# Kernel optimization log

Hardware: AMD Instinct MI355X
Metric: run time of the kernel (lower is better)

## Reference

```python
import jax, jax.numpy as jnp
import numpy as np

D_MODEL = 2048
NUM_HEADS = 16
HEAD_DIM = D_MODEL // NUM_HEADS
BATCH = 2
SEQ = 2048


def setup_inputs() -> dict:
    key = jax.random.key(0)
    ks = jax.random.split(key, 5)
    scale = 1.0 / np.sqrt(D_MODEL)
    x = jax.random.normal(ks[0], (BATCH, SEQ, D_MODEL), dtype=jnp.float32)
    wq = jax.random.normal(ks[1], (D_MODEL, D_MODEL), dtype=jnp.float32) * scale
    wk = jax.random.normal(ks[2], (D_MODEL, D_MODEL), dtype=jnp.float32) * scale
    wv = jax.random.normal(ks[3], (D_MODEL, D_MODEL), dtype=jnp.float32) * scale
    wo = jax.random.normal(ks[4], (D_MODEL, D_MODEL), dtype=jnp.float32) * scale
    return {"x": x, "wq": wq, "wk": wk, "wv": wv, "wo": wo}


def reference(x, wq, wk, wv, wo):
    # x: [B, S, D_MODEL]; torch nn.Linear(bias=False): y = x @ W.T
    B, S, _ = x.shape

    def split_heads(t):
        # [B, S, D] -> [B, H, S, Dh]
        return t.reshape(B, S, NUM_HEADS, HEAD_DIM).transpose(0, 2, 1, 3)

    q = split_heads(x @ wq.T)
    k = split_heads(x @ wk.T)
    v = split_heads(x @ wv.T)

    # scaled dot-product attention with causal (tril) mask, single-rank path
    scores = jnp.einsum("bhqd,bhkd->bhqk", q, k) / jnp.sqrt(
        jnp.asarray(HEAD_DIM, dtype=x.dtype)
    )
    causal = jnp.tril(jnp.ones((S, S), dtype=bool))  # [S, S]
    neg_inf = jnp.asarray(jnp.finfo(scores.dtype).min, dtype=scores.dtype)
    scores = jnp.where(causal[None, None, :, :], scores, neg_inf)
    attn = jax.nn.softmax(scores, axis=-1)

    out = jnp.einsum("bhqk,bhkd->bhqd", attn, v)  # [B, H, S, Dh]
    out = out.transpose(0, 2, 1, 3).reshape(B, S, D_MODEL)
    return out @ wo.T
```

## Files before the change

### kernel.cpp

```cpp
#include <hip/hip_runtime.h>
#include <hip/hip_bf16.h>

#define D_MODEL   2048
#define NUM_HEADS 16
#define HEAD_DIM  128
#define BATCH     2
#define SEQ       2048

typedef short bf16x8 __attribute__((ext_vector_type(8)));
typedef float f32x4  __attribute__((ext_vector_type(4)));

__device__ inline short f2bf(float x) {
    __hip_bfloat16 h = __float2bfloat16(x);
    return *reinterpret_cast<short*>(&h);
}

__device__ inline void async_copy16(const void* g, void* l) {
    __builtin_amdgcn_global_load_lds(
        (const __attribute__((address_space(1))) void*)g,
        (__attribute__((address_space(3))) void*)l, 16, 0, 0);
}
__device__ inline void wait_all() { __builtin_amdgcn_s_waitcnt(0); }

__global__ __launch_bounds__(256) void f32_to_bf16(
    const float* __restrict__ src, __hip_bfloat16* __restrict__ dst, int n8) {
    const int i = blockIdx.x * 256 + threadIdx.x;
    if (i >= n8) return;
    const f32x4* p = (const f32x4*)src + (size_t)i * 2;
    f32x4 f0 = p[0], f1 = p[1];
    bf16x8 v;
#pragma unroll
    for (int j = 0; j < 4; ++j) { v[j] = f2bf(f0[j]); v[4 + j] = f2bf(f1[j]); }
    *(bf16x8*)((short*)dst + (size_t)i * 8) = v;
}

__global__ __launch_bounds__(256) void cvt5(
    const float* __restrict__ x,  __hip_bfloat16* __restrict__ xb,
    const float* __restrict__ w0, __hip_bfloat16* __restrict__ w0b,
    const float* __restrict__ w1, __hip_bfloat16* __restrict__ w1b,
    const float* __restrict__ w2, __hip_bfloat16* __restrict__ w2b,
    const float* __restrict__ w3, __hip_bfloat16* __restrict__ w3b) {
    const int b = blockIdx.x;
    const float* src; short* dst; int idx;
    if (b < 4096)       { src = x;  dst = (short*)xb;  idx = b; }
    else if (b < 6144)  { src = w0; dst = (short*)w0b; idx = b - 4096; }
    else if (b < 8192)  { src = w1; dst = (short*)w1b; idx = b - 6144; }
    else if (b < 10240) { src = w2; dst = (short*)w2b; idx = b - 8192; }
    else                { src = w3; dst = (short*)w3b; idx = b - 10240; }
    const int i = idx * 256 + threadIdx.x;
    const f32x4* p = (const f32x4*)src + (size_t)i * 2;
    f32x4 f0 = p[0], f1 = p[1];
    bf16x8 v;
#pragma unroll
    for (int j = 0; j < 4; ++j) { v[j] = f2bf(f0[j]); v[4 + j] = f2bf(f1[j]); }
    *(bf16x8*)(dst + (size_t)i * 8) = v;
}

template <bool OUT_F32>
__global__ __launch_bounds__(256) void gemm_v4(
    const __hip_bfloat16* __restrict__ A,
    const __hip_bfloat16* __restrict__ W0,
    const __hip_bfloat16* __restrict__ W1,
    const __hip_bfloat16* __restrict__ W2,
    void* __restrict__ C0, void* __restrict__ C1, void* __restrict__ C2,
    int M, int N, int K) {
    __shared__ short As[2][128 * 64];
    __shared__ short Ws[2][128 * 64];

    const int z = blockIdx.z;
    const __hip_bfloat16* W = (z == 0) ? W0 : (z == 1) ? W1 : W2;
    void* Cv = (z == 0) ? C0 : (z == 1) ? C1 : C2;

    const int gx  = gridDim.x;
    const int nwg = gx * gridDim.y;
    const int wg  = blockIdx.y * gx + blockIdx.x;
    const int swz = (wg & 7) * (nwg >> 3) + (wg >> 3);
    const int bx  = swz % gx;
    const int by  = swz / gx;

    const int tid  = threadIdx.x;
    const int lane = tid & 63;
    const int wv   = tid >> 6;
    const int c    = lane & 15;
    const int quad = lane >> 4;
    const int m0   = by * 128;
    const int n0   = bx * 128;
    const int wm   = (wv >> 1) * 64;
    const int wn   = (wv & 1) * 64;

    f32x4 acc[4][4];
#pragma unroll
    for (int mi = 0; mi < 4; ++mi)
#pragma unroll
        for (int ni = 0; ni < 4; ++ni)
            acc[mi][ni] = (f32x4){0.f, 0.f, 0.f, 0.f};

    const char* ga[4];
    const char* gw[4];
    int lo[4];
#pragma unroll
    for (int i = 0; i < 4; ++i) {
        const int o   = (i * 256 + tid) * 16;
        const int row = o >> 7;
        const int sc  = (o & 127) ^ ((row & 7) << 4);
        ga[i] = (const char*)(A + (size_t)(m0 + row) * K) + sc;
        gw[i] = (const char*)(W + (size_t)(n0 + row) * K) + sc;
        lo[i] = o;
    }

    const int nt = K >> 6;

#pragma unroll
    for (int i = 0; i < 4; ++i) {
        async_copy16(ga[i], (char*)As[0] + lo[i]);
        async_copy16(gw[i], (char*)Ws[0] + lo[i]);
    }
    __syncthreads();

    int cur = 0;
    for (int t = 0; t < nt; ++t) {
        if (t + 1 < nt) {
            const size_t kb = (size_t)(t + 1) << 7;
#pragma unroll
            for (int i = 0; i < 4; ++i) {
                async_copy16(ga[i] + kb, (char*)As[cur ^ 1] + lo[i]);
                async_copy16(gw[i] + kb, (char*)Ws[cur ^ 1] + lo[i]);
            }
        }

        const short* Asc = As[cur];
        const short* Wsc = Ws[cur];
#pragma unroll
        for (int ks = 0; ks < 2; ++ks) {
            bf16x8 a[4], b[4];
#pragma unroll
            for (int mi = 0; mi < 4; ++mi) {
                const int r = wm + mi * 16 + c;
                a[mi] = *(const bf16x8*)((const char*)Asc + r * 128 +
                                         ((ks * 64 + quad * 16) ^ ((r & 7) << 4)));
            }
#pragma unroll
            for (int ni = 0; ni < 4; ++ni) {
                const int r = wn + ni * 16 + c;
                b[ni] = *(const bf16x8*)((const char*)Wsc + r * 128 +
                                         ((ks * 64 + quad * 16) ^ ((r & 7) << 4)));
            }
            __builtin_amdgcn_s_setprio(1);
#pragma unroll
            for (int mi = 0; mi < 4; ++mi)
#pragma unroll
                for (int ni = 0; ni < 4; ++ni)
                    acc[mi][ni] = __builtin_amdgcn_mfma_f32_16x16x32_bf16(
                        a[mi], b[ni], acc[mi][ni], 0, 0, 0);
            __builtin_amdgcn_s_setprio(0);
        }
        __syncthreads();
        cur ^= 1;
    }

#pragma unroll
    for (int mi = 0; mi < 4; ++mi)
#pragma unroll
        for (int ni = 0; ni < 4; ++ni)
#pragma unroll
            for (int r = 0; r < 4; ++r) {
                const int m = m0 + wm + mi * 16 + quad * 4 + r;
                const int n = n0 + wn + ni * 16 + c;
                if (OUT_F32)
                    ((float*)Cv)[(size_t)m * N + n] = acc[mi][ni][r];
                else
                    ((__hip_bfloat16*)Cv)[(size_t)m * N + n] = __float2bfloat16(acc[mi][ni][r]);
            }
}

__global__ __launch_bounds__(256) void transpose2k(
    const __hip_bfloat16* __restrict__ Vin, __hip_bfloat16* __restrict__ Vout) {
    __shared__ short T[64 * 72];
    const int tid = threadIdx.x;
    const int d0  = blockIdx.x * 64;
    const int s0  = blockIdx.y * 64;
    const size_t half = (size_t)SEQ * D_MODEL;
    const short* in  = (const short*)Vin + blockIdx.z * half;
    short*       out = (short*)Vout      + blockIdx.z * half;

#pragma unroll
    for (int i = 0; i < 2; ++i) {
        const int lin = i * 256 + tid;
        const int sr  = lin >> 3;
        const int sg  = lin & 7;
        *(uint4*)&T[sr * 72 + sg * 8] =
            *(const uint4*)&in[(size_t)(s0 + sr) * D_MODEL + d0 + sg * 8];
    }
    __syncthreads();
#pragma unroll
    for (int i = 0; i < 2; ++i) {
        const int lin = i * 256 + tid;
        const int dr  = lin >> 3;
        const int sg  = lin & 7;
        bf16x8 v;
#pragma unroll
        for (int j = 0; j < 8; ++j) v[j] = T[(sg * 8 + j) * 72 + dr];
        *(uint4*)&out[(size_t)(d0 + dr) * SEQ + s0 + sg * 8] = *(uint4*)&v;
    }
}

__global__ __launch_bounds__(256) void attn_v8(
    const __hip_bfloat16* Qg,
    const __hip_bfloat16* __restrict__ Kg,
    const __hip_bfloat16* __restrict__ Vt,
    __hip_bfloat16* Og) {
    constexpr int LDP = 72;
    __shared__ short Ks[2][64 * 128];
    __shared__ short Vs[2][128 * 64];
    __shared__ __hip_bfloat16 Pl[64 * LDP];

    const int tid  = threadIdx.x;
    const int lane = tid & 63;
    const int w    = tid >> 6;
    const int c    = lane & 15;
    const int quad = lane >> 4;
    const int qlo  = blockIdx.x;
    const int qhi  = (SEQ / 64 - 1) - qlo;
    const int h    = blockIdx.y;
    const size_t half = (size_t)SEQ * D_MODEL;
    const __hip_bfloat16* Qb  = Qg + blockIdx.z * half;
    const __hip_bfloat16* Kb  = Kg + blockIdx.z * half;
    const __hip_bfloat16* Vtb = Vt + blockIdx.z * half;
    __hip_bfloat16*       Ob  = Og + blockIdx.z * half;
    const size_t base = (size_t)h * HEAD_DIM;
    const int prow0 = w * 16;
    const float scale = 0.08838834764831845f;

    for (int pass = 0; pass < 2; ++pass) {
        const int myq = pass ? qlo : qhi;
        const int q0  = myq * 64;
        const int wq0 = q0 + prow0;

        __syncthreads();

        bf16x8 qf[4];
#pragma unroll
        for (int kk = 0; kk < 4; ++kk)
            qf[kk] = *(const bf16x8*)((const short*)Qb + base +
                                      (size_t)(wq0 + c) * D_MODEL + kk * 32 + quad * 8);

        float l_run[4] = {0.f, 0.f, 0.f, 0.f};
        f32x4 o_acc[8];
#pragma unroll
        for (int dt = 0; dt < 8; ++dt) o_acc[dt] = (f32x4){0.f, 0.f, 0.f, 0.f};

#pragma unroll
        for (int i = 0; i < 4; ++i) {
            const int o = (i * 256 + tid) * 16;
            {
                const int row = o >> 8, colb = o & 255;
                const int scol = colb ^ ((row & 7) << 4);
                async_copy16((const char*)(Kb + base + (size_t)row * D_MODEL) + scol,
                             (char*)Ks[0] + o);
            }
            {
                const int row = o >> 7, colb = o & 127;
                const int scol = colb ^ ((row & 7) << 4);
                async_copy16((const char*)(Vtb + (size_t)(base + row) * SEQ) + scol,
                             (char*)Vs[0] + o);
            }
        }

        int cur = 0;
        const int nch = myq + 1;
        for (int ch = 0; ch < nch; ++ch) {
            __syncthreads();

            if (ch + 1 < nch) {
                const int key0n = (ch + 1) * 64;
#pragma unroll
                for (int i = 0; i < 4; ++i) {
                    const int o = (i * 256 + tid) * 16;
                    {
                        const int row = o >> 8, colb = o & 255;
                        const int scol = colb ^ ((row & 7) << 4);
                        async_copy16((const char*)(Kb + base + (size_t)(key0n + row) * D_MODEL) + scol,
                                     (char*)Ks[cur ^ 1] + o);
                    }
                    {
                        const int row = o >> 7, colb = o & 127;
                        const int scol = colb ^ ((row & 7) << 4);
                        async_copy16((const char*)(Vtb + (size_t)(base + row) * SEQ + key0n) + scol,
                                     (char*)Vs[cur ^ 1] + o);
                    }
                }
            }

            const int key0 = ch * 64;
            const short* Ksc = Ks[cur];
            const short* Vsc = Vs[cur];
            f32x4 s[4];
#pragma unroll
            for (int kt = 0; kt < 4; ++kt) s[kt] = (f32x4){0.f, 0.f, 0.f, 0.f};
            __builtin_amdgcn_s_setprio(1);
#pragma unroll
            for (int kk = 0; kk < 4; ++kk)
#pragma unroll
                for (int kt = 0; kt < 4; ++kt) {
                    const int r  = kt * 16 + c;
                    const int cb = (kk * 64 + quad * 16) ^ ((r & 7) << 4);
                    bf16x8 kf = *(const bf16x8*)((const char*)Ksc + r * 256 + cb);
                    s[kt] = __builtin_amdgcn_mfma_f32_16x16x32_bf16(qf[kk], kf, s[kt], 0, 0, 0);
                }
            __builtin_amdgcn_s_setprio(0);

            const bool diag = (ch == myq);
#pragma unroll
            for (int r = 0; r < 4; ++r) {
                const int qg = wq0 + quad * 4 + r;
                const int lrow = prow0 + quad * 4 + r;
                float p[4], rs = 0.f;
#pragma unroll
                for (int kt = 0; kt < 4; ++kt) {
                    float v = s[kt][r] * scale;
                    if (diag && (key0 + kt * 16 + c > qg)) v = -1e30f;
                    p[kt] = __expf(v);
                    rs += p[kt];
                }
#pragma unroll
                for (int off = 1; off < 16; off <<= 1)
                    rs += __shfl_xor(rs, off);
                l_run[r] += rs;
#pragma unroll
                for (int kt = 0; kt < 4; ++kt)
                    Pl[lrow * LDP + kt * 16 + c] = __float2bfloat16(p[kt]);
            }

#pragma unroll
            for (int kk = 0; kk < 2; ++kk) {
                bf16x8 pa = *(const bf16x8*)((const short*)Pl +
                                             (prow0 + c) * LDP + kk * 32 + quad * 8);
                __builtin_amdgcn_s_setprio(1);
#pragma unroll
                for (int dt = 0; dt < 8; ++dt) {
                    const int rv  = dt * 16 + c;
                    const int cbv = (kk * 64 + quad * 16) ^ ((rv & 7) << 4);
                    bf16x8 vb = *(const bf16x8*)((const char*)Vsc + rv * 128 + cbv);
                    o_acc[dt] = __builtin_amdgcn_mfma_f32_16x16x32_bf16(pa, vb, o_acc[dt], 0, 0, 0);
                }
                __builtin_amdgcn_s_setprio(0);
            }

            cur ^= 1;
        }

#pragma unroll
        for (int r = 0; r < 4; ++r) {
            const float inv = 1.0f / l_run[r];
            const int row = wq0 + quad * 4 + r;
#pragma unroll
            for (int dt = 0; dt < 8; ++dt)
                Ob[base + (size_t)row * D_MODEL + dt * 16 + c] =
                    __float2bfloat16(o_acc[dt][r] * inv);
        }
    }
}

template <bool A_F32, bool W_F32, bool OUT_F32>
__global__ __launch_bounds__(256) void gemm_bt(
    const void* __restrict__ Av, const void* __restrict__ Wv,
    void* __restrict__ Cv, int M, int N, int K) {
    __shared__ __hip_bfloat16 As[128 * 32];
    __shared__ __hip_bfloat16 Ws[128 * 32];
    const int tid = threadIdx.x, lane = tid & 63, wv = tid >> 6;
    const int c = lane & 15, quad = lane >> 4;
    const int m0 = blockIdx.y * 128, n0 = blockIdx.x * 128;
    const int wm = (wv >> 1) * 64, wn = (wv & 1) * 64;
    f32x4 acc[4][4];
#pragma unroll
    for (int mi = 0; mi < 4; ++mi)
#pragma unroll
        for (int ni = 0; ni < 4; ++ni) acc[mi][ni] = (f32x4){0.f, 0.f, 0.f, 0.f};
    const int nk = K >> 5;
    for (int kb = 0; kb < nk; ++kb) {
        __syncthreads();
#pragma unroll
        for (int i = 0; i < 2; ++i) {
            const int e = (i * 256 + tid) * 8;
            const int row = e >> 5, col = e & 31;
            if (A_F32) {
                const float* p = (const float*)Av + (size_t)(m0 + row) * K + kb * 32 + col;
                f32x4 f0 = *(const f32x4*)p, f1 = *(const f32x4*)(p + 4);
                bf16x8 v;
#pragma unroll
                for (int j = 0; j < 4; ++j) { v[j] = f2bf(f0[j]); v[4 + j] = f2bf(f1[j]); }
                *(bf16x8*)((short*)As + e) = v;
            } else {
                *(uint4*)((short*)As + e) =
                    *(const uint4*)((const short*)Av + (size_t)(m0 + row) * K + kb * 32 + col);
            }
            if (W_F32) {
                const float* p = (const float*)Wv + (size_t)(n0 + row) * K + kb * 32 + col;
                f32x4 f0 = *(const f32x4*)p, f1 = *(const f32x4*)(p + 4);
                bf16x8 v;
#pragma unroll
                for (int j = 0; j < 4; ++j) { v[j] = f2bf(f0[j]); v[4 + j] = f2bf(f1[j]); }
                *(bf16x8*)((short*)Ws + e) = v;
            } else {
                *(uint4*)((short*)Ws + e) =
                    *(const uint4*)((const short*)Wv + (size_t)(n0 + row) * K + kb * 32 + col);
            }
        }
        __syncthreads();
        bf16x8 a[4], b[4];
#pragma unroll
        for (int mi = 0; mi < 4; ++mi)
            a[mi] = *(const bf16x8*)((const short*)As + (wm + mi * 16 + c) * 32 + quad * 8);
#pragma unroll
        for (int ni = 0; ni < 4; ++ni)
            b[ni] = *(const bf16x8*)((const short*)Ws + (wn + ni * 16 + c) * 32 + quad * 8);
#pragma unroll
        for (int mi = 0; mi < 4; ++mi)
#pragma unroll
            for (int ni = 0; ni < 4; ++ni)
                acc[mi][ni] = __builtin_amdgcn_mfma_f32_16x16x32_bf16(a[mi], b[ni], acc[mi][ni], 0, 0, 0);
    }
#pragma unroll
    for (int mi = 0; mi < 4; ++mi)
#pragma unroll
        for (int ni = 0; ni < 4; ++ni)
#pragma unroll
            for (int r = 0; r < 4; ++r) {
                const int m = m0 + wm + mi * 16 + quad * 4 + r;
                const int n = n0 + wn + ni * 16 + c;
                if (OUT_F32) ((float*)Cv)[(size_t)m * N + n] = acc[mi][ni][r];
                else ((__hip_bfloat16*)Cv)[(size_t)m * N + n] = __float2bfloat16(acc[mi][ni][r]);
            }
}

__global__ __launch_bounds__(256) void attn_fused_v2(
    const __hip_bfloat16* Qg, const __hip_bfloat16* __restrict__ Kg,
    const __hip_bfloat16* __restrict__ Vg, __hip_bfloat16* Og) {
    constexpr int LDK = 136, LDP = 72;
    __shared__ __hip_bfloat16 Kc[64 * LDK];
    __shared__ __hip_bfloat16 Vc[64 * LDK];
    __shared__ __hip_bfloat16 Pl[64 * LDP];
    __shared__ float alpha_l[64];
    __shared__ float l_l[64];
    const int tid = threadIdx.x, lane = tid & 63, w = tid >> 6;
    const int c = lane & 15, quad = lane >> 4;
    const int qb = blockIdx.x, h = blockIdx.y;
    const size_t base = (size_t)h * HEAD_DIM;
    const int q0 = qb * 64, wq0 = q0 + w * 16, dt0 = w * 2;
    bf16x8 qf[4];
#pragma unroll
    for (int kk = 0; kk < 4; ++kk)
        qf[kk] = *(const bf16x8*)((const short*)Qg + base +
                                  (size_t)(wq0 + c) * D_MODEL + kk * 32 + quad * 8);
    float m_run[4], l_run[4];
#pragma unroll
    for (int r = 0; r < 4; ++r) { m_run[r] = -1e30f; l_run[r] = 0.f; }
    f32x4 o_acc[4][2];
#pragma unroll
    for (int qt = 0; qt < 4; ++qt)
#pragma unroll
        for (int dd = 0; dd < 2; ++dd) o_acc[qt][dd] = (f32x4){0.f, 0.f, 0.f, 0.f};
    const float scale = 0.08838834764831845f;
    const int nch = qb + 1;
    for (int ch = 0; ch < nch; ++ch) {
        const int key0 = ch * 64;
        __syncthreads();
#pragma unroll
        for (int i = 0; i < 4; ++i) {
            const int lin = i * 256 + tid;
            const int kr = lin >> 4, cg = lin & 15;
            *(uint4*)((short*)Kc + kr * LDK + cg * 8) =
                *(const uint4*)&Kg[base + (size_t)(key0 + kr) * D_MODEL + cg * 8];
            *(uint4*)((short*)Vc + kr * LDK + cg * 8) =
                *(const uint4*)&Vg[base + (size_t)(key0 + kr) * D_MODEL + cg * 8];
        }
        __syncthreads();
        f32x4 s[4];
#pragma unroll
        for (int kt = 0; kt < 4; ++kt) s[kt] = (f32x4){0.f, 0.f, 0.f, 0.f};
#pragma unroll
        for (int kk = 0; kk < 4; ++kk)
#pragma unroll
            for (int kt = 0; kt < 4; ++kt) {
                bf16x8 kb = *(const bf16x8*)((const short*)Kc + (kt * 16 + c) * LDK + kk * 32 + quad * 8);
                s[kt] = __builtin_amdgcn_mfma_f32_16x16x32_bf16(qf[kk], kb, s[kt], 0, 0, 0);
            }
#pragma unroll
        for (int r = 0; r < 4; ++r) {
            const int qg = wq0 + quad * 4 + r;
            float v[4];
#pragma unroll
            for (int kt = 0; kt < 4; ++kt) {
                v[kt] = s[kt][r] * scale;
                if (key0 + kt * 16 + c > qg) v[kt] = -1e30f;
            }
            float mx = fmaxf(fmaxf(v[0], v[1]), fmaxf(v[2], v[3]));
#pragma unroll
            for (int off = 1; off < 16; off <<= 1) mx = fmaxf(mx, __shfl_xor(mx, off));
            const float m_new = fmaxf(m_run[r], mx);
            const float al = __expf(m_run[r] - m_new);
            float p[4], rs = 0.f;
#pragma unroll
            for (int kt = 0; kt < 4; ++kt) { p[kt] = __expf(v[kt] - m_new); rs += p[kt]; }
#pragma unroll
            for (int off = 1; off < 16; off <<= 1) rs += __shfl_xor(rs, off);
            l_run[r] = l_run[r] * al + rs;
            m_run[r] = m_new;
            const int lrow = w * 16 + quad * 4 + r;
#pragma unroll
            for (int kt = 0; kt < 4; ++kt) Pl[lrow * LDP + kt * 16 + c] = __float2bfloat16(p[kt]);
            if (c == 0) alpha_l[lrow] = al;
        }
        __syncthreads();
#pragma unroll
        for (int qt = 0; qt < 4; ++qt)
#pragma unroll
            for (int r = 0; r < 4; ++r) {
                const float al = alpha_l[qt * 16 + quad * 4 + r];
                o_acc[qt][0][r] *= al;
                o_acc[qt][1][r] *= al;
            }
#pragma unroll
        for (int kk = 0; kk < 2; ++kk) {
            bf16x8 pa[4];
#pragma unroll
            for (int qt = 0; qt < 4; ++qt)
                pa[qt] = *(const bf16x8*)((const short*)Pl + (qt * 16 + c) * LDP + kk * 32 + quad * 8);
#pragma unroll
            for (int dd = 0; dd < 2; ++dd) {
                bf16x8 vb;
#pragma unroll
                for (int j = 0; j < 8; ++j)
                    vb[j] = ((const short*)Vc)[(kk * 32 + quad * 8 + j) * LDK + (dt0 + dd) * 16 + c];
#pragma unroll
                for (int qt = 0; qt < 4; ++qt)
                    o_acc[qt][dd] = __builtin_amdgcn_mfma_f32_16x16x32_bf16(pa[qt], vb, o_acc[qt][dd], 0, 0, 0);
            }
        }
    }
    if (c == 0)
#pragma unroll
        for (int r = 0; r < 4; ++r) l_l[w * 16 + quad * 4 + r] = l_run[r];
    __syncthreads();
#pragma unroll
    for (int qt = 0; qt < 4; ++qt)
#pragma unroll
        for (int r = 0; r < 4; ++r) {
            const float inv = 1.0f / l_l[qt * 16 + quad * 4 + r];
            const int row = q0 + qt * 16 + quad * 4 + r;
#pragma unroll
            for (int dd = 0; dd < 2; ++dd)
                Og[base + (size_t)row * D_MODEL + (dt0 + dd) * 16 + c] =
                    __float2bfloat16(o_acc[qt][dd][r] * inv);
        }
}

extern "C" void kernel_launch(void* const* d_in, const int* in_sizes, int n_in,
                              void* d_out, int out_size, void* d_ws, size_t ws_size,
                              hipStream_t stream) {
    const float* x  = (const float*)d_in[0];
    const float* wq = (const float*)d_in[1];
    const float* wk = (const float*)d_in[2];
    const float* wv = (const float*)d_in[3];
    const float* wo = (const float*)d_in[4];
    float* out = (float*)d_out;

    const size_t half  = (size_t)SEQ * D_MODEL;
    const size_t WELEM = (size_t)D_MODEL * D_MODEL;
    const size_t needA = (4 * WELEM + 5 * 2 * half) * 2;
    const size_t needB = (4 * WELEM + 4 * half) * 2;

    if (ws_size >= needA) {
        __hip_bfloat16* wqb = (__hip_bfloat16*)d_ws;
        __hip_bfloat16* wkb = wqb + WELEM;
        __hip_bfloat16* wvb = wkb + WELEM;
        __hip_bfloat16* wob = wvb + WELEM;
        __hip_bfloat16* xb  = wob + WELEM;
        __hip_bfloat16* Q   = xb + 2 * half;
        __hip_bfloat16* Kf  = Q  + 2 * half;
        __hip_bfloat16* Vf  = Kf + 2 * half;
        __hip_bfloat16* Vt  = xb;

        cvt5<<<12288, 256, 0, stream>>>(x, xb, wq, wqb, wk, wkb, wv, wvb, wo, wob);

        gemm_v4<false><<<dim3(16, 32, 3), 256, 0, stream>>>(
            xb, wqb, wkb, wvb, Q, Kf, Vf, 4096, D_MODEL, D_MODEL);
        transpose2k<<<dim3(32, 32, 2), 256, 0, stream>>>(Vf, Vt);
        attn_v8<<<dim3(16, 16, 2), 256, 0, stream>>>(Q, Kf, Vt, Q);
        gemm_v4<true><<<dim3(16, 32, 1), 256, 0, stream>>>(
            Q, wob, wob, wob, out, out, out, 4096, D_MODEL, D_MODEL);
    } else if (ws_size >= needB) {
        __hip_bfloat16* wqb = (__hip_bfloat16*)d_ws;
        __hip_bfloat16* wkb = wqb + WELEM;
        __hip_bfloat16* wvb = wkb + WELEM;
        __hip_bfloat16* wob = wvb + WELEM;
        __hip_bfloat16* xbb = wob + WELEM;
        __hip_bfloat16* Qb  = xbb + half;
        __hip_bfloat16* Kb  = Qb + half;
        __hip_bfloat16* Vb  = Kb + half;
        __hip_bfloat16* Vtb = xbb;

        f32_to_bf16<<<2048, 256, 0, stream>>>(wq, wqb, (int)(WELEM / 8));
        f32_to_bf16<<<2048, 256, 0, stream>>>(wk, wkb, (int)(WELEM / 8));
        f32_to_bf16<<<2048, 256, 0, stream>>>(wv, wvb, (int)(WELEM / 8));
        f32_to_bf16<<<2048, 256, 0, stream>>>(wo, wob, (int)(WELEM / 8));
        for (int b = 0; b < BATCH; ++b) {
            f32_to_bf16<<<2048, 256, 0, stream>>>(x + b * half, xbb, (int)(half / 8));
            gemm_v4<false><<<dim3(16, 16, 3), 256, 0, stream>>>(
                xbb, wqb, wkb, wvb, Qb, Kb, Vb, 2048, D_MODEL, D_MODEL);
            transpose2k<<<dim3(32, 32, 1), 256, 0, stream>>>(Vb, Vtb);
            attn_v8<<<dim3(16, 16, 1), 256, 0, stream>>>(Qb, Kb, Vtb, Qb);
            gemm_v4<true><<<dim3(16, 16, 1), 256, 0, stream>>>(
                Qb, wob, wob, wob, out + b * half, out, out, 2048, D_MODEL, D_MODEL);
        }
    } else {
        __hip_bfloat16* Qb = (__hip_bfloat16*)d_ws;
        __hip_bfloat16* Kb = Qb + half;
        __hip_bfloat16* Vb = Kb + half;
        dim3 gg(16, 16);
        dim3 ga(32, 16);
        for (int b = 0; b < BATCH; ++b) {
            const float* xbp = x + b * half;
            gemm_bt<true, true, false><<<gg, 256, 0, stream>>>(xbp, wq, Qb, 2048, D_MODEL, D_MODEL);
            gemm_bt<true, true, false><<<gg, 256, 0, stream>>>(xbp, wk, Kb, 2048, D_MODEL, D_MODEL);
            gemm_bt<true, true, false><<<gg, 256, 0, stream>>>(xbp, wv, Vb, 2048, D_MODEL, D_MODEL);
            attn_fused_v2<<<ga, 256, 0, stream>>>(Qb, Kb, Vb, Qb);
            gemm_bt<false, true, true><<<gg, 256, 0, stream>>>(Qb, wo, out + b * half, 2048, D_MODEL, D_MODEL);
        }
    }
}
```

Baseline: 375.7 us.

## Triple-buffer GEMM K-loop with BK=32 and remap attention block indices

The GEMM now uses three LDS stages of 32-wide K tiles, prefetching two tiles ahead. A single partial vmcnt wait plus one barrier per iteration replaces the two full syncs around each 64-wide tile. This is meant to hide global-to-LDS latency and shrink LDS use, at the cost of more loop iterations and fewer MFMAs per barrier. The attention launch is flattened to a 1D grid whose block-to-(head, batch, q-tile) mapping places heads and batches so that 8 adjacent blocks share a q-tile pair across heads, which may change cache and XCD locality.

```diff
diff --git a/kernel.cpp b/kernel.cpp
--- a/kernel.cpp
+++ b/kernel.cpp
@@ -20,7 +20,6 @@
         (const __attribute__((address_space(1))) void*)g,
         (__attribute__((address_space(3))) void*)l, 16, 0, 0);
 }
-__device__ inline void wait_all() { __builtin_amdgcn_s_waitcnt(0); }
 
 __global__ __launch_bounds__(256) void f32_to_bf16(
     const float* __restrict__ src, __hip_bfloat16* __restrict__ dst, int n8) {
@@ -57,15 +56,15 @@
 }
 
 template <bool OUT_F32>
-__global__ __launch_bounds__(256) void gemm_v4(
+__global__ __launch_bounds__(256) void gemm_v5(
     const __hip_bfloat16* __restrict__ A,
     const __hip_bfloat16* __restrict__ W0,
     const __hip_bfloat16* __restrict__ W1,
     const __hip_bfloat16* __restrict__ W2,
     void* __restrict__ C0, void* __restrict__ C1, void* __restrict__ C2,
     int M, int N, int K) {
-    __shared__ short As[2][128 * 64];
-    __shared__ short Ws[2][128 * 64];
+    __shared__ short As[3][128 * 32];
+    __shared__ short Ws[3][128 * 32];
 
     const int z = blockIdx.z;
     const __hip_bfloat16* W = (z == 0) ? W0 : (z == 1) ? W1 : W2;
@@ -95,67 +94,73 @@
         for (int ni = 0; ni < 4; ++ni)
             acc[mi][ni] = (f32x4){0.f, 0.f, 0.f, 0.f};
 
-    const char* ga[4];
-    const char* gw[4];
-    int lo[4];
-#pragma unroll
-    for (int i = 0; i < 4; ++i) {
+    const char* ga[2];
+    const char* gw[2];
+    int lo[2];
+#pragma unroll
+    for (int i = 0; i < 2; ++i) {
         const int o   = (i * 256 + tid) * 16;
-        const int row = o >> 7;
-        const int sc  = (o & 127) ^ ((row & 7) << 4);
+        const int row = o >> 6;
+        const int sc  = (o & 63) ^ ((row & 3) << 4);
         ga[i] = (const char*)(A + (size_t)(m0 + row) * K) + sc;
         gw[i] = (const char*)(W + (size_t)(n0 + row) * K) + sc;
         lo[i] = o;
     }
 
-    const int nt = K >> 6;
-
-#pragma unroll
-    for (int i = 0; i < 4; ++i) {
+    const int nt = K >> 5;
+
+#pragma unroll
+    for (int i = 0; i < 2; ++i) {
         async_copy16(ga[i], (char*)As[0] + lo[i]);
         async_copy16(gw[i], (char*)Ws[0] + lo[i]);
     }
-    __syncthreads();
+#pragma unroll
+    for (int i = 0; i < 2; ++i) {
+        async_copy16(ga[i] + 64, (char*)As[1] + lo[i]);
+        async_copy16(gw[i] + 64, (char*)Ws[1] + lo[i]);
+    }
 
     int cur = 0;
     for (int t = 0; t < nt; ++t) {
-        if (t + 1 < nt) {
-            const size_t kb = (size_t)(t + 1) << 7;
-#pragma unroll
-            for (int i = 0; i < 4; ++i) {
-                async_copy16(ga[i] + kb, (char*)As[cur ^ 1] + lo[i]);
-                async_copy16(gw[i] + kb, (char*)Ws[cur ^ 1] + lo[i]);
+        asm volatile("s_waitcnt vmcnt(4)" ::: "memory");
+        __builtin_amdgcn_s_barrier();
+        __builtin_amdgcn_sched_barrier(0);
+
+        if (t + 2 < nt) {
+            int nb = cur + 2; if (nb >= 3) nb -= 3;
+            const size_t kb = (size_t)(t + 2) << 6;
+#pragma unroll
+            for (int i = 0; i < 2; ++i) {
+                async_copy16(ga[i] + kb, (char*)As[nb] + lo[i]);
+                async_copy16(gw[i] + kb, (char*)Ws[nb] + lo[i]);
             }
         }
 
         const short* Asc = As[cur];
         const short* Wsc = Ws[cur];
-#pragma unroll
-        for (int ks = 0; ks < 2; ++ks) {
-            bf16x8 a[4], b[4];
-#pragma unroll
-            for (int mi = 0; mi < 4; ++mi) {
-                const int r = wm + mi * 16 + c;
-                a[mi] = *(const bf16x8*)((const char*)Asc + r * 128 +
-                                         ((ks * 64 + quad * 16) ^ ((r & 7) << 4)));
-            }
-#pragma unroll
-            for (int ni = 0; ni < 4; ++ni) {
-                const int r = wn + ni * 16 + c;
-                b[ni] = *(const bf16x8*)((const char*)Wsc + r * 128 +
-                                         ((ks * 64 + quad * 16) ^ ((r & 7) << 4)));
-            }
-            __builtin_amdgcn_s_setprio(1);
-#pragma unroll
-            for (int mi = 0; mi < 4; ++mi)
-#pragma unroll
-                for (int ni = 0; ni < 4; ++ni)
-                    acc[mi][ni] = __builtin_amdgcn_mfma_f32_16x16x32_bf16(
-                        a[mi], b[ni], acc[mi][ni], 0, 0, 0);
-            __builtin_amdgcn_s_setprio(0);
-        }
-        __syncthreads();
-        cur ^= 1;
+        bf16x8 a[4], b[4];
+#pragma unroll
+        for (int mi = 0; mi < 4; ++mi) {
+            const int r = wm + mi * 16 + c;
+            a[mi] = *(const bf16x8*)((const char*)Asc + r * 64 +
+                                     ((quad * 16) ^ ((r & 3) << 4)));
+        }
+#pragma unroll
+        for (int ni = 0; ni < 4; ++ni) {
+            const int r = wn + ni * 16 + c;
+            b[ni] = *(const bf16x8*)((const char*)Wsc + r * 64 +
+                                     ((quad * 16) ^ ((r & 3) << 4)));
+        }
+        __builtin_amdgcn_s_setprio(1);
+#pragma unroll
+        for (int mi = 0; mi < 4; ++mi)
+#pragma unroll
+            for (int ni = 0; ni < 4; ++ni)
+                acc[mi][ni] = __builtin_amdgcn_mfma_f32_16x16x32_bf16(
+                    a[mi], b[ni], acc[mi][ni], 0, 0, 0);
+        __builtin_amdgcn_s_setprio(0);
+
+        cur += 1; if (cur >= 3) cur -= 3;
     }
 
 #pragma unroll
@@ -204,7 +209,7 @@
     }
 }
 
-__global__ __launch_bounds__(256) void attn_v8(
+__global__ __launch_bounds__(256) void attn_v9(
     const __hip_bfloat16* Qg,
     const __hip_bfloat16* __restrict__ Kg,
     const __hip_bfloat16* __restrict__ Vt,
@@ -214,19 +219,23 @@
     __shared__ short Vs[2][128 * 64];
     __shared__ __hip_bfloat16 Pl[64 * LDP];
 
+    const int bid  = blockIdx.x;
+    const int qlo  = (bid >> 3) & 15;
+    const int qhi  = (SEQ / 64 - 1) - qlo;
+    const int hb   = (bid & 7) + 8 * (bid >> 7);
+    const int h    = hb & (NUM_HEADS - 1);
+    const int bz   = hb >> 4;
+
     const int tid  = threadIdx.x;
     const int lane = tid & 63;
     const int w    = tid >> 6;
     const int c    = lane & 15;
     const int quad = lane >> 4;
-    const int qlo  = blockIdx.x;
-    const int qhi  = (SEQ / 64 - 1) - qlo;
-    const int h    = blockIdx.y;
     const size_t half = (size_t)SEQ * D_MODEL;
-    const __hip_bfloat16* Qb  = Qg + blockIdx.z * half;
-    const __hip_bfloat16* Kb  = Kg + blockIdx.z * half;
-    const __hip_bfloat16* Vtb = Vt + blockIdx.z * half;
-    __hip_bfloat16*       Ob  = Og + blockIdx.z * half;
+    const __hip_bfloat16* Qb  = Qg + bz * half;
+    const __hip_bfloat16* Kb  = Kg + bz * half;
+    const __hip_bfloat16* Vtb = Vt + bz * half;
+    __hip_bfloat16*       Ob  = Og + bz * half;
     const size_t base = (size_t)h * HEAD_DIM;
     const int prow0 = w * 16;
     const float scale = 0.08838834764831845f;
@@ -583,11 +592,11 @@
 
         cvt5<<<12288, 256, 0, stream>>>(x, xb, wq, wqb, wk, wkb, wv, wvb, wo, wob);
 
-        gemm_v4<false><<<dim3(16, 32, 3), 256, 0, stream>>>(
+        gemm_v5<false><<<dim3(16, 32, 3), 256, 0, stream>>>(
             xb, wqb, wkb, wvb, Q, Kf, Vf, 4096, D_MODEL, D_MODEL);
         transpose2k<<<dim3(32, 32, 2), 256, 0, stream>>>(Vf, Vt);
-        attn_v8<<<dim3(16, 16, 2), 256, 0, stream>>>(Q, Kf, Vt, Q);
-        gemm_v4<true><<<dim3(16, 32, 1), 256, 0, stream>>>(
+        attn_v9<<<512, 256, 0, stream>>>(Q, Kf, Vt, Q);
+        gemm_v5<true><<<dim3(16, 32, 1), 256, 0, stream>>>(
             Q, wob, wob, wob, out, out, out, 4096, D_MODEL, D_MODEL);
     } else if (ws_size >= needB) {
         __hip_bfloat16* wqb = (__hip_bfloat16*)d_ws;
@@ -606,11 +615,11 @@
         f32_to_bf16<<<2048, 256, 0, stream>>>(wo, wob, (int)(WELEM / 8));
         for (int b = 0; b < BATCH; ++b) {
             f32_to_bf16<<<2048, 256, 0, stream>>>(x + b * half, xbb, (int)(half / 8));
-            gemm_v4<false><<<dim3(16, 16, 3), 256, 0, stream>>>(
+            gemm_v5<false><<<dim3(16, 16, 3), 256, 0, stream>>>(
                 xbb, wqb, wkb, wvb, Qb, Kb, Vb, 2048, D_MODEL, D_MODEL);
             transpose2k<<<dim3(32, 32, 1), 256, 0, stream>>>(Vb, Vtb);
-            attn_v8<<<dim3(16, 16, 1), 256, 0, stream>>>(Qb, Kb, Vtb, Qb);
-            gemm_v4<true><<<dim3(16, 16, 1), 256, 0, stream>>>(
+            attn_v9<<<256, 256, 0, stream>>>(Qb, Kb, Vtb, Qb);
+            gemm_v5<true><<<dim3(16, 16, 1), 256, 0, stream>>>(
                 Qb, wob, wob, wob, out + b * half, out, out, 2048, D_MODEL, D_MODEL);
         }
     } else {
```

After: 374.2 us. Within noise of the previous version (-0.4%).
